# Kernel tuning notes

Measured on AMD Instinct MI355X. Metric: run time of the kernel, lower is better.

## Reference

```python
import jax, jax.numpy as jnp
import numpy as np

K_NN = 20  # neighbors per group (k=20 in source)


def fps_one(xyz, npoint):
    # xyz: [N,3] -> indices [npoint] via iterative furthest point sampling
    N = xyz.shape[0]
    def body(carry, _):
        dist, far = carry
        d = jnp.sum((xyz - xyz[far]) ** 2, axis=-1)
        dist = jnp.minimum(dist, d)
        return (dist, jnp.argmax(dist).astype(jnp.int32)), far
    init = (jnp.full((N,), 1e10, xyz.dtype), jnp.int32(0))
    _, idx = jax.lax.scan(body, init, None, length=npoint)
    return idx


def gather(pts, idx):
    # pts: [B,M,C], idx: [B,...] -> [B,...,C]
    return jax.vmap(lambda p, i: p[i])(pts, idx)


def knn(q, ref, k):
    # q: [B,S,3], ref: [B,M,3] -> [B,S,k] indices of nearest refs
    d = (jnp.sum(q * q, -1, keepdims=True)
         - 2.0 * jnp.einsum('bsc,bmc->bsm', q, ref)
         + jnp.sum(ref * ref, -1)[:, None, :])
    _, idx = jax.lax.top_k(-d, k)
    return idx


def sa_block(xyz, feats, npoint, W, b):
    # Set abstraction: FPS sample -> kNN group -> shared MLP -> max pool
    fidx = jax.vmap(fps_one, in_axes=(0, None))(xyz, npoint)   # [B,S]
    new_xyz = gather(xyz, fidx)                                 # [B,S,3]
    nidx = knn(new_xyz, xyz, K_NN)                              # [B,S,K]
    rel = gather(xyz, nidx) - new_xyz[:, :, None, :]            # [B,S,K,3]
    grp = jnp.concatenate([rel, gather(feats, nidx)], -1)       # [B,S,K,3+C]
    h = jax.nn.relu(jnp.einsum('bskc,cd->bskd', grp, W) + b)
    return new_xyz, jnp.max(h, axis=2)                          # [B,S,Cout]


def fp_block(xq, xr, fr, skip, W, b):
    # Feature propagation: 3-NN inverse-distance interp -> concat skip -> MLP
    idx = knn(xq, xr, 3)                                        # [B,S,3]
    d = jnp.sum((gather(xr, idx) - xq[:, :, None, :]) ** 2, -1)
    w = 1.0 / (d + 1e-8)
    w = w / jnp.sum(w, -1, keepdims=True)
    interp = jnp.einsum('bsk,bskc->bsc', w, gather(fr, idx))
    cat = jnp.concatenate([interp, skip], -1)
    return jax.nn.relu(jnp.einsum('bsc,cd->bsd', cat, W) + b)


def setup_inputs() -> dict:
    key = jax.random.key(0)
    ks = jax.random.split(key, 24)
    B, N = 8, 4096
    x = jax.random.normal(ks[0], (B, 6, N), jnp.float32)
    cls_label = jax.random.uniform(ks[1], (B, 16), jnp.float32)
    def lin(k, cin, cout):
        kw, kb = jax.random.split(k)
        s = 1.0 / np.sqrt(cin)
        return (jax.random.normal(kw, (cin, cout), jnp.float32) * s,
                jax.random.normal(kb, (cout,), jnp.float32) * 0.01)
    W0, b0 = lin(ks[2], 6, 64)
    W1, b1 = lin(ks[3], 67, 128)
    W2, b2 = lin(ks[4], 131, 256)
    W3, b3 = lin(ks[5], 259, 512)
    F3, fb3 = lin(ks[6], 768, 512)
    F2, fb2 = lin(ks[7], 640, 256)
    F1, fb1 = lin(ks[8], 320, 128)
    F0, fb0 = lin(ks[9], 150, 128)
    Wseg, bseg = lin(ks[10], 128, 50)
    return {"x": x, "cls_label": cls_label,
            "W0": W0, "b0": b0, "W1": W1, "b1": b1, "W2": W2, "b2": b2,
            "W3": W3, "b3": b3, "F3": F3, "fb3": fb3, "F2": F2, "fb2": fb2,
            "F1": F1, "fb1": fb1, "F0": F0, "fb0": fb0,
            "Wseg": Wseg, "bseg": bseg}


def reference(x, cls_label, W0, b0, W1, b1, W2, b2, W3, b3,
              F3, fb3, F2, fb2, F1, fb1, F0, fb0, Wseg, bseg):
    B, _, N = x.shape
    xyz = jnp.transpose(x[:, :3, :], (0, 2, 1))   # [B,N,3]
    nrm = jnp.transpose(x[:, 3:, :], (0, 2, 1))   # [B,N,3]
    # hierarchical set abstraction (512 -> 256 -> 128 -> 64 points)
    x1, f1 = sa_block(xyz, nrm, 512, W0, b0)      # f1: [B,512,64]
    x2, f2 = sa_block(x1, f1, 256, W1, b1)        # f2: [B,256,128]
    x3, f3 = sa_block(x2, f2, 128, W2, b2)        # f3: [B,128,256]
    x4, f4 = sa_block(x3, f3, 64, W3, b3)         # f4: [B,64,512]
    # feature propagation back up
    g3 = fp_block(x3, x4, f4, f3, F3, fb3)        # [B,128,512]
    g2 = fp_block(x2, x3, g3, f2, F2, fb2)        # [B,256,256]
    g1 = fp_block(x1, x2, g2, f1, F1, fb1)        # [B,512,128]
    cls = jnp.broadcast_to(cls_label[:, None, :], (B, N, 16))
    skip0 = jnp.concatenate([cls, xyz, nrm], -1)  # [B,N,22]
    g0 = fp_block(xyz, x1, g1, skip0, F0, fb0)    # [B,N,128]
    result = jnp.einsum('bnc,cd->bnd', g0, Wseg) + bseg  # [B,N,50]
    return result, jnp.transpose(g0, (0, 2, 1))
```

## Files before the change

### kernel.cpp

```cpp
#include <hip/hip_runtime.h>
#include <float.h>

#define B8 8
#define NPTS 4096

__global__ void split_xyz_kernel(const float* __restrict__ x,
                                 float* __restrict__ xyz, float* __restrict__ nrm) {
  int g = blockIdx.x * 256 + threadIdx.x;
  if (g >= B8 * NPTS) return;
  int b = g / NPTS, n = g % NPTS;
  const float* xb = x + (size_t)b * 6 * NPTS;
  float* o1 = xyz + (size_t)g * 3;
  float* o2 = nrm + (size_t)g * 3;
  o1[0] = xb[0 * NPTS + n]; o1[1] = xb[1 * NPTS + n]; o1[2] = xb[2 * NPTS + n];
  o2[0] = xb[3 * NPTS + n]; o2[1] = xb[4 * NPTS + n]; o2[2] = xb[5 * NPTS + n];
}

template <int CTRL, int RM>
__device__ __forceinline__ unsigned dppmov(unsigned v) {
  return (unsigned)__builtin_amdgcn_update_dpp((int)v, (int)v, CTRL, RM, 0xf, false);
}

template <int CTRL, int RM>
__device__ __forceinline__ void red_key_max(unsigned& kh, unsigned& kl) {
  unsigned oh = dppmov<CTRL, RM>(kh);
  unsigned ol = dppmov<CTRL, RM>(kl);
  unsigned long long ko = ((unsigned long long)oh << 32) | ol;
  unsigned long long k  = ((unsigned long long)kh << 32) | kl;
  bool c = ko > k;
  kh = c ? oh : kh;
  kl = c ? ol : kl;
}

template <int CTRL, int RM>
__device__ __forceinline__ void red_key_min(unsigned& kh, unsigned& kl) {
  unsigned oh = dppmov<CTRL, RM>(kh);
  unsigned ol = dppmov<CTRL, RM>(kl);
  unsigned long long ko = ((unsigned long long)oh << 32) | ol;
  unsigned long long k  = ((unsigned long long)kh << 32) | kl;
  bool c = ko < k;
  kh = c ? oh : kh;
  kl = c ? ol : kl;
}

#define WAVE_RED_MAX(kh, kl)            \
  red_key_max<0x111, 0xf>(kh, kl);      \
  red_key_max<0x112, 0xf>(kh, kl);      \
  red_key_max<0x114, 0xf>(kh, kl);      \
  red_key_max<0x118, 0xf>(kh, kl);      \
  red_key_max<0x142, 0xa>(kh, kl);      \
  red_key_max<0x143, 0xc>(kh, kl);

#define WAVE_RED_MIN(kh, kl)            \
  red_key_min<0x111, 0xf>(kh, kl);      \
  red_key_min<0x112, 0xf>(kh, kl);      \
  red_key_min<0x114, 0xf>(kh, kl);      \
  red_key_min<0x118, 0xf>(kh, kl);      \
  red_key_min<0x142, 0xa>(kh, kl);      \
  red_key_min<0x143, 0xc>(kh, kl);

template <int BLOCK, int P>
__global__ __launch_bounds__(BLOCK) void fps4_kernel(const float* __restrict__ xyz,
                                                     int N, int S,
                                                     float* __restrict__ out_xyz) {
#pragma clang fp contract(off)
  constexpr int NW = BLOCK / 64;
  __shared__ float4 pts[BLOCK * P];
  __shared__ float4 sel[512];
  __shared__ alignas(16) unsigned long long wkey[2][NW];
  int b = blockIdx.x, t = threadIdx.x;
  const float* p = xyz + (size_t)b * N * 3;
  float px[P], py[P], pz[P], dist[P];
#pragma unroll
  for (int j = 0; j < P; ++j) {
    int idx = t + j * BLOCK;
    float a = p[3 * idx], bb = p[3 * idx + 1], c = p[3 * idx + 2];
    px[j] = a; py[j] = bb; pz[j] = c;
    pts[idx] = make_float4(a, bb, c, 0.f);
    dist[j] = 1e10f;
  }
  __syncthreads();
  float fx = p[0], fy = p[1], fz = p[2];
  for (int i = 0; i < S; ++i) {
    if (t == 0) sel[i] = make_float4(fx, fy, fz, 0.f);
    float bv = -1.0f;
    int bj = 0;
#pragma unroll
    for (int j = 0; j < P; ++j) {
      float dx = px[j] - fx, dy = py[j] - fy, dz = pz[j] - fz;
      float d = dx * dx + dy * dy + dz * dz;
      float nd = fminf(dist[j], d);
      dist[j] = nd;
      bool c = nd > bv;
      bv = c ? nd : bv;
      bj = c ? j : bj;
    }
    unsigned kh = __float_as_uint(bv);
    unsigned kl = (unsigned)(~(t + bj * BLOCK));
    WAVE_RED_MAX(kh, kl);
    int buf = i & 1;
    if ((t & 63) == 63)
      wkey[buf][t >> 6] = ((unsigned long long)kh << 32) | kl;
    __syncthreads();
    unsigned long long g = 0ull;
    const ulonglong2* wk2 = (const ulonglong2*)&wkey[buf][0];
#pragma unroll
    for (int w = 0; w < NW / 2; ++w) {
      ulonglong2 e = wk2[w];
      unsigned long long m = (e.x > e.y) ? e.x : e.y;
      g = (m > g) ? m : g;
    }
    int far = (int)~(unsigned)g;
    float4 f = pts[far];
    fx = f.x; fy = f.y; fz = f.z;
  }
  __syncthreads();
  for (int i = t; i < S; i += BLOCK) {
    float4 f = sel[i];
    float* o = out_xyz + ((size_t)b * S + i) * 3;
    o[0] = f.x; o[1] = f.y; o[2] = f.z;
  }
}

__global__ __launch_bounds__(64) void knn20_kernel(const float* __restrict__ q,
                                                   const float* __restrict__ ref,
                                                   int S, int M, int* __restrict__ nidx,
                                                   int LDQ, int LDR) {
#pragma clang fp contract(off)
  int bs = blockIdx.x;
  int b = bs / S, s = bs % S;
  int t = threadIdx.x;
  __shared__ float sd[4096];
  const float* qp = q + ((size_t)b * LDQ + s) * 3;
  float qx = qp[0], qy = qp[1], qz = qp[2];
  float qq = qx * qx + qy * qy + qz * qz;
  const float* rp = ref + (size_t)b * LDR * 3;
  for (int i = t; i < M; i += 64) {
    float rx = rp[3 * i], ry = rp[3 * i + 1], rz = rp[3 * i + 2];
    float rr = rx * rx + ry * ry + rz * rz;
    float dot = qx * rx + qy * ry + qz * rz;
    sd[i] = qq - 2.0f * dot + rr;
  }
  __syncthreads();
  unsigned keep = 0;
  for (int k = 0; k < 20; ++k) {
    float bv = FLT_MAX;
    int bi = 0;
    for (int i = t; i < M; i += 64) {
      float v = sd[i];
      bool c = v < bv;
      bv = c ? v : bv;
      bi = c ? i : bi;
    }
    unsigned kh = __float_as_uint(bv), kl = (unsigned)bi;
    WAVE_RED_MIN(kh, kl);
    unsigned w = (unsigned)__builtin_amdgcn_readlane((int)kl, 63);
    if (t == k) keep = w;
    if (t == 0) sd[w] = FLT_MAX;
    __syncthreads();
  }
  if (t < 20) nidx[(size_t)bs * 20 + t] = (int)keep;
}

__device__ __forceinline__ void knn3_store(int g, const float* rx3,
                                           float qx, float qy, float qz,
                                           int i0, int i1, int i2,
                                           int* __restrict__ idx3,
                                           float* __restrict__ w3) {
#pragma clang fp contract(off)
  int ii[3] = {i0, i1, i2};
  float w[3];
  float wsum = 0.0f;
#pragma unroll
  for (int k = 0; k < 3; ++k) {
    const float* r = rx3 + (size_t)ii[k] * 3;
    float dx = r[0] - qx, dy = r[1] - qy, dz = r[2] - qz;
    float d = dx * dx + dy * dy + dz * dz;
    w[k] = 1.0f / (d + 1e-8f);
    wsum += w[k];
  }
#pragma unroll
  for (int k = 0; k < 3; ++k) {
    idx3[(size_t)g * 3 + k] = ii[k];
    w3[(size_t)g * 3 + k] = w[k] / wsum;
  }
}

__global__ __launch_bounds__(256) void neighbors_kernel(
    const float* __restrict__ xyz, const float* __restrict__ x1,
    int* __restrict__ nidx2, int* __restrict__ nidx3, int* __restrict__ nidx4,
    int* __restrict__ idx3_3, float* __restrict__ w3_3,
    int* __restrict__ idx3_2, float* __restrict__ w3_2,
    int* __restrict__ idx3_1, float* __restrict__ w3_1,
    int* __restrict__ idx3_0, float* __restrict__ w3_0) {
#pragma clang fp contract(off)
  __shared__ float4 smem4[512];
  int blk = blockIdx.x, tid = threadIdx.x;

  if (blk < 896) {
    int S, M, qid;
    int* nout;
    const int wv = tid >> 6, t64 = tid & 63;
    if (blk < 512)      { S = 256; M = 512; qid = blk * 4 + wv;         nout = nidx2; }
    else if (blk < 768) { S = 128; M = 256; qid = (blk - 512) * 4 + wv; nout = nidx3; }
    else                { S = 64;  M = 128; qid = (blk - 768) * 4 + wv; nout = nidx4; }
    float* swd = (float*)smem4 + wv * M;
    int b = qid / S, s = qid % S;
    const float* qp = x1 + ((size_t)b * 512 + s) * 3;
    float qx = qp[0], qy = qp[1], qz = qp[2];
    float qq = qx * qx + qy * qy + qz * qz;
    const float* rp = x1 + (size_t)b * 512 * 3;
    for (int i = t64; i < M; i += 64) {
      float rx = rp[3 * i], ry = rp[3 * i + 1], rz = rp[3 * i + 2];
      float rr = rx * rx + ry * ry + rz * rz;
      float dot = qx * rx + qy * ry + qz * rz;
      swd[i] = qq - 2.0f * dot + rr;
    }
    __syncthreads();
    unsigned keep = 0;
    for (int k = 0; k < 20; ++k) {
      float bv = FLT_MAX;
      int bi = 0;
      for (int i = t64; i < M; i += 64) {
        float v = swd[i];
        bool c = v < bv;
        bv = c ? v : bv;
        bi = c ? i : bi;
      }
      unsigned kh = __float_as_uint(bv), kl = (unsigned)bi;
      WAVE_RED_MIN(kh, kl);
      unsigned w = (unsigned)__builtin_amdgcn_readlane((int)kl, 63);
      if (t64 == k) keep = w;
      if (t64 == 0) swd[w] = FLT_MAX;
      __syncthreads();
    }
    if (t64 < 20) nout[(size_t)qid * 20 + t64] = (int)keep;
    return;
  }

  if (blk < 900) {
    int g = (blk - 896) * 256 + tid;
    int Sq = 128, M = 64;
    int b = g / Sq, s = g % Sq;
    const float* qp = x1 + ((size_t)b * 512 + s) * 3;
    float qx = qp[0], qy = qp[1], qz = qp[2];
    float qq = qx * qx + qy * qy + qz * qz;
    const float* rp = x1 + (size_t)b * 512 * 3;
    float v0 = FLT_MAX, v1 = FLT_MAX, v2 = FLT_MAX;
    int i0 = 0, i1 = 0, i2 = 0;
    for (int i = 0; i < M; ++i) {
      float rx = rp[3 * i], ry = rp[3 * i + 1], rz = rp[3 * i + 2];
      float d = qq - 2.0f * (qx * rx + qy * ry + qz * rz) + (rx * rx + ry * ry + rz * rz);
      if (d < v2) {
        if (d < v1) {
          if (d < v0) { v2 = v1; i2 = i1; v1 = v0; i1 = i0; v0 = d; i0 = i; }
          else { v2 = v1; i2 = i1; v1 = d; i1 = i; }
        } else { v2 = d; i2 = i; }
      }
    }
    knn3_store(g, rp, qx, qy, qz, i0, i1, i2, idx3_3, w3_3);
    return;
  }

  int g, Sq, M, LDQ;
  int* oidx;
  float* ow;
  const float* q;
  if (blk < 908)      { g = (blk - 900) * 256 + tid; Sq = 256;  M = 128; oidx = idx3_2; ow = w3_2; q = x1;  LDQ = 512; }
  else if (blk < 924) { g = (blk - 908) * 256 + tid; Sq = 512;  M = 256; oidx = idx3_1; ow = w3_1; q = x1;  LDQ = 512; }
  else                { g = (blk - 924) * 256 + tid; Sq = 4096; M = 512; oidx = idx3_0; ow = w3_0; q = xyz; LDQ = 4096; }
  int b = g / Sq, s = g % Sq;
  const float* rp = x1 + (size_t)b * 512 * 3;
  for (int i = tid; i < M; i += 256) {
    float rx = rp[3 * i], ry = rp[3 * i + 1], rz = rp[3 * i + 2];
    smem4[i] = make_float4(rx, ry, rz, rx * rx + ry * ry + rz * rz);
  }
  __syncthreads();
  const float* qp = q + ((size_t)b * LDQ + s) * 3;
  float qx = qp[0], qy = qp[1], qz = qp[2];
  float qq = qx * qx + qy * qy + qz * qz;
  float v0 = FLT_MAX, v1 = FLT_MAX, v2 = FLT_MAX;
  int i0 = 0, i1 = 0, i2 = 0;
  for (int i = 0; i < M; ++i) {
    float4 r = smem4[i];
    float d = qq - 2.0f * (qx * r.x + qy * r.y + qz * r.z) + r.w;
    if (d < v2) {
      if (d < v1) {
        if (d < v0) { v2 = v1; i2 = i1; v1 = v0; i1 = i0; v0 = d; i0 = i; }
        else { v2 = v1; i2 = i1; v1 = d; i1 = i; }
      } else { v2 = d; i2 = i; }
    }
  }
  {
    int ii[3] = {i0, i1, i2};
    float w[3];
    float wsum = 0.0f;
#pragma unroll
    for (int k = 0; k < 3; ++k) {
      float4 r = smem4[ii[k]];
      float dx = r.x - qx, dy = r.y - qy, dz = r.z - qz;
      float d = dx * dx + dy * dy + dz * dz;
      w[k] = 1.0f / (d + 1e-8f);
      wsum += w[k];
    }
#pragma unroll
    for (int k = 0; k < 3; ++k) {
      oidx[(size_t)g * 3 + k] = ii[k];
      ow[(size_t)g * 3 + k] = w[k] / wsum;
    }
  }
}

#define GEMM_STAGE(k0v, ...)                                                      \
    _Pragma("unroll")                                                             \
    for (int u = 0; u < 4; ++u) {                                                 \
      int l = (int)threadIdx.x + u * 256;                                         \
      int m = l >> 4, kk = l & 15;                                                \
      int rr = rowBase + m, kq = (k0v) + kk;                                      \
      float v = 0.0f;                                                             \
      if (rr < Mrows && kq < K) { __VA_ARGS__ }                                   \
      areg[u] = v;                                                                \
    }                                                                             \
    _Pragma("unroll")                                                             \
    for (int u = 0; u < 4; ++u) {                                                 \
      int l = (int)threadIdx.x + u * 256;                                         \
      int kk = l >> 6, n = l & 63;                                                \
      int kq = (k0v) + kk, cc = colBase + n;                                      \
      breg[u] = (kq < K && cc < N) ? Wm[(size_t)kq * N + cc] : 0.0f;              \
    }

#define GEMM_WRITE_LDS(bufv)                                                      \
    _Pragma("unroll")                                                             \
    for (int u = 0; u < 4; ++u) {                                                 \
      int l = (int)threadIdx.x + u * 256;                                         \
      As[bufv][l & 15][l >> 4] = areg[u];                                         \
    }                                                                             \
    _Pragma("unroll")                                                             \
    for (int u = 0; u < 4; ++u) {                                                 \
      int l = (int)threadIdx.x + u * 256;                                         \
      Bs[bufv][l >> 6][l & 63] = breg[u];                                         \
    }

#define GEMM_MAIN(...)                                                            \
  __shared__ alignas(16) float As[2][16][68];                                     \
  __shared__ float Bs[2][16][64];                                                 \
  int tx = threadIdx.x & 15, ty = threadIdx.x >> 4;                               \
  int rowBase = blockIdx.y * 64;                                                  \
  int colBase = blockIdx.x * 64;                                                  \
  float acc[4][4] = {};                                                           \
  float areg[4], breg[4];                                                         \
  GEMM_STAGE(0, __VA_ARGS__)                                                      \
  GEMM_WRITE_LDS(0)                                                               \
  __syncthreads();                                                                \
  int cur = 0;                                                                    \
  for (int k0 = 0; k0 < K; k0 += 16) {                                            \
    int nxt = cur ^ 1;                                                            \
    bool more = (k0 + 16 < K);                                                    \
    if (more) { GEMM_STAGE(k0 + 16, __VA_ARGS__) }                                \
    _Pragma("unroll")                                                             \
    for (int kk = 0; kk < 16; ++kk) {                                             \
      const float4 av = *reinterpret_cast<const float4*>(&As[cur][kk][ty * 4]);   \
      const float4 bv = *reinterpret_cast<const float4*>(&Bs[cur][kk][tx * 4]);   \
      acc[0][0] += av.x * bv.x; acc[0][1] += av.x * bv.y;                         \
      acc[0][2] += av.x * bv.z; acc[0][3] += av.x * bv.w;                         \
      acc[1][0] += av.y * bv.x; acc[1][1] += av.y * bv.y;                         \
      acc[1][2] += av.y * bv.z; acc[1][3] += av.y * bv.w;                         \
      acc[2][0] += av.z * bv.x; acc[2][1] += av.z * bv.y;                         \
      acc[2][2] += av.z * bv.z; acc[2][3] += av.z * bv.w;                         \
      acc[3][0] += av.w * bv.x; acc[3][1] += av.w * bv.y;                         \
      acc[3][2] += av.w * bv.z; acc[3][3] += av.w * bv.w;                         \
    }                                                                             \
    if (more) { GEMM_WRITE_LDS(nxt) }                                             \
    __syncthreads();                                                              \
    cur = nxt;                                                                    \
  }

#define GEMM_EPI_STORE                                                            \
  _Pragma("unroll")                                                               \
  for (int i = 0; i < 4; ++i) {                                                   \
    int row = rowBase + ty * 4 + i;                                               \
    if (row >= Mrows) continue;                                                   \
    _Pragma("unroll")                                                             \
    for (int j = 0; j < 4; ++j) {                                                 \
      int col = colBase + tx * 4 + j;                                             \
      if (col >= N) continue;                                                     \
      float v = acc[i][j] + bias[col];                                            \
      if (RELU) v = fmaxf(v, 0.0f);                                               \
      C[(size_t)row * N + col] = v;                                               \
    }                                                                             \
  }

__global__ __launch_bounds__(256) void gemm_kernel(const float* __restrict__ A,
                                                   const float* __restrict__ Wm,
                                                   const float* __restrict__ bias,
                                                   float* __restrict__ C,
                                                   int Mrows, int N, int K, int RELU) {
  GEMM_MAIN( v = A[(size_t)rr * K + kq]; )
  GEMM_EPI_STORE
}

__global__ __launch_bounds__(256) void gemm_sa_kernel(
    const float* __restrict__ xyz, const float* __restrict__ feats,
    const float* __restrict__ new_xyz, const int* __restrict__ nidx,
    const float* __restrict__ Wm, const float* __restrict__ bias,
    float* __restrict__ fOut, int Mref, int LDR, int S, int LDQ, int Cf,
    int Mrows, int N, int K) {
  GEMM_MAIN(
    int bs = rr / 20;
    int s_ = bs % S;
    int b = bs / S;
    int id = nidx[rr];
    if (kq < 3)
      v = xyz[((size_t)b * LDR + id) * 3 + kq] - new_xyz[((size_t)b * LDQ + s_) * 3 + kq];
    else
      v = feats[((size_t)b * Mref + id) * Cf + (kq - 3)];
  )
  __shared__ int smax[4][64];
  int gBase = rowBase / 20;
  int nG = (rowBase + 63) / 20 - gBase + 1;
  for (int l = threadIdx.x; l < nG * 64; l += 256) smax[l >> 6][l & 63] = 0;
  __syncthreads();
#pragma unroll
  for (int i = 0; i < 4; ++i) {
    int row = rowBase + ty * 4 + i;
    if (row >= Mrows) continue;
    int gl = row / 20 - gBase;
#pragma unroll
    for (int j = 0; j < 4; ++j) {
      int col = colBase + tx * 4 + j;
      if (col >= N) continue;
      float v = fmaxf(acc[i][j] + bias[col], 0.0f);
      atomicMax(&smax[gl][col - colBase], __float_as_int(v));
    }
  }
  __syncthreads();
  for (int l = threadIdx.x; l < nG * 64; l += 256) {
    int g = gBase + (l >> 6), c = colBase + (l & 63);
    if (c < N) atomicMax((int*)&fOut[(size_t)g * N + c], smax[l >> 6][l & 63]);
  }
}

__global__ __launch_bounds__(256) void gemm_fp_kernel(
    const float* __restrict__ fr, const int* __restrict__ idx3,
    const float* __restrict__ w3, const float* __restrict__ skip,
    const float* __restrict__ cls, const float* __restrict__ xyzq,
    const float* __restrict__ nrmq,
    const float* __restrict__ Wm, const float* __restrict__ bias,
    float* __restrict__ C, int Sq, int Mr, int Cr, int Cs, int mode,
    int Mrows, int N, int K) {
  const int RELU = 1;
  GEMM_MAIN(
    int bs = rr;
    int b = bs / Sq;
    if (kq < Cr) {
      const int* ii = idx3 + (size_t)bs * 3;
      const float* ww = w3 + (size_t)bs * 3;
      const float* fb = fr + (size_t)b * Mr * Cr;
      v = ww[0] * fb[(size_t)ii[0] * Cr + kq];
      v += ww[1] * fb[(size_t)ii[1] * Cr + kq];
      v += ww[2] * fb[(size_t)ii[2] * Cr + kq];
    } else {
      int cc = kq - Cr;
      if (mode == 0) {
        v = skip[(size_t)bs * Cs + cc];
      } else {
        if (cc < 16) v = cls[(size_t)b * 16 + cc];
        else if (cc < 19) v = xyzq[(size_t)bs * 3 + (cc - 16)];
        else v = nrmq[(size_t)bs * 3 + (cc - 19)];
      }
    }
  )
  GEMM_EPI_STORE
}

__global__ __launch_bounds__(256) void transpose_g0_kernel(const float* __restrict__ g0,
                                                           float* __restrict__ out2) {
  __shared__ float tile[32][33];
  int n0 = blockIdx.x * 32, c0 = blockIdx.y * 32, b = blockIdx.z;
  int tx = threadIdx.x & 31, ty = threadIdx.x >> 5;
#pragma unroll
  for (int j = 0; j < 32; j += 8)
    tile[ty + j][tx] = g0[((size_t)b * NPTS + n0 + ty + j) * 128 + c0 + tx];
  __syncthreads();
#pragma unroll
  for (int j = 0; j < 32; j += 8)
    out2[((size_t)b * 128 + c0 + ty + j) * NPTS + n0 + tx] = tile[tx][ty + j];
}

static inline int cdiv(int a, int b) { return (a + b - 1) / b; }

extern "C" void kernel_launch(void* const* d_in, const int* in_sizes, int n_in,
                              void* d_out, int out_size, void* d_ws, size_t ws_size,
                              hipStream_t stream) {
  const float* x    = (const float*)d_in[0];
  const float* cls  = (const float*)d_in[1];
  const float* W0 = (const float*)d_in[2];  const float* b0 = (const float*)d_in[3];
  const float* W1 = (const float*)d_in[4];  const float* b1 = (const float*)d_in[5];
  const float* W2 = (const float*)d_in[6];  const float* b2 = (const float*)d_in[7];
  const float* W3 = (const float*)d_in[8];  const float* b3 = (const float*)d_in[9];
  const float* F3 = (const float*)d_in[10]; const float* fb3 = (const float*)d_in[11];
  const float* F2 = (const float*)d_in[12]; const float* fb2 = (const float*)d_in[13];
  const float* F1 = (const float*)d_in[14]; const float* fb1 = (const float*)d_in[15];
  const float* F0 = (const float*)d_in[16]; const float* fb0 = (const float*)d_in[17];
  const float* Wseg = (const float*)d_in[18]; const float* bseg = (const float*)d_in[19];
  float* out = (float*)d_out;

  float* ws = (float*)d_ws;
  size_t off = 0;
  auto alloc = [&](size_t n) { float* p = ws + off; off += (n + 3) & ~(size_t)3; return p; };
  float* xyz = alloc(8 * 4096 * 3);
  float* nrm = alloc(8 * 4096 * 3);
  float* x1 = alloc(8 * 512 * 3);
  float* f1 = alloc(8 * 512 * 64);
  float* f2 = alloc(8 * 256 * 128);
  float* f3 = alloc(8 * 128 * 256);
  float* f4 = alloc(8 * 64 * 512);
  float* g3 = alloc(8 * 128 * 512);
  float* g2 = alloc(8 * 256 * 256);
  float* g1 = alloc(8 * 512 * 128);
  float* g0 = alloc(8 * 4096 * 128);
  int* nidx1 = (int*)alloc(8 * 512 * 20);
  int* nidx2 = (int*)alloc(8 * 256 * 20);
  int* nidx3 = (int*)alloc(8 * 128 * 20);
  int* nidx4 = (int*)alloc(8 * 64 * 20);
  int* idx3_3 = (int*)alloc(8 * 128 * 3);  float* w3_3 = alloc(8 * 128 * 3);
  int* idx3_2 = (int*)alloc(8 * 256 * 3);  float* w3_2 = alloc(8 * 256 * 3);
  int* idx3_1 = (int*)alloc(8 * 512 * 3);  float* w3_1 = alloc(8 * 512 * 3);
  int* idx3_0 = (int*)alloc(8 * 4096 * 3); float* w3_0 = alloc(8 * 4096 * 3);

  hipMemsetAsync(f1, 0, (size_t)8 * (512 * 64 + 256 * 128 + 128 * 256 + 64 * 512) * 4, stream);

  split_xyz_kernel<<<cdiv(8 * 4096, 256), 256, 0, stream>>>(x, xyz, nrm);
  fps4_kernel<256, 16><<<8, 256, 0, stream>>>(xyz, 4096, 512, x1);
  knn20_kernel<<<8 * 512, 64, 0, stream>>>(x1, xyz, 512, 4096, nidx1, 512, 4096);
  neighbors_kernel<<<1052, 256, 0, stream>>>(xyz, x1, nidx2, nidx3, nidx4,
                                             idx3_3, w3_3, idx3_2, w3_2,
                                             idx3_1, w3_1, idx3_0, w3_0);

  {
    dim3 grid(1, cdiv(8 * 512 * 20, 64));
    gemm_sa_kernel<<<grid, 256, 0, stream>>>(xyz, nrm, x1, nidx1, W0, b0, f1,
                                             4096, 4096, 512, 512, 3,
                                             8 * 512 * 20, 64, 6);
  }
  {
    dim3 grid(2, cdiv(8 * 256 * 20, 64));
    gemm_sa_kernel<<<grid, 256, 0, stream>>>(x1, f1, x1, nidx2, W1, b1, f2,
                                             512, 512, 256, 512, 64,
                                             8 * 256 * 20, 128, 67);
  }
  {
    dim3 grid(4, cdiv(8 * 128 * 20, 64));
    gemm_sa_kernel<<<grid, 256, 0, stream>>>(x1, f2, x1, nidx3, W2, b2, f3,
                                             256, 512, 128, 512, 128,
                                             8 * 128 * 20, 256, 131);
  }
  {
    dim3 grid(8, cdiv(8 * 64 * 20, 64));
    gemm_sa_kernel<<<grid, 256, 0, stream>>>(x1, f3, x1, nidx4, W3, b3, f4,
                                             128, 512, 64, 512, 256,
                                             8 * 64 * 20, 512, 259);
  }

  {
    dim3 grid(8, cdiv(8 * 128, 64));
    gemm_fp_kernel<<<grid, 256, 0, stream>>>(f4, idx3_3, w3_3, f3, nullptr, nullptr, nullptr,
                                             F3, fb3, g3, 128, 64, 512, 256, 0,
                                             8 * 128, 512, 768);
  }
  {
    dim3 grid(4, cdiv(8 * 256, 64));
    gemm_fp_kernel<<<grid, 256, 0, stream>>>(g3, idx3_2, w3_2, f2, nullptr, nullptr, nullptr,
                                             F2, fb2, g2, 256, 128, 512, 128, 0,
                                             8 * 256, 256, 640);
  }
  {
    dim3 grid(2, cdiv(8 * 512, 64));
    gemm_fp_kernel<<<grid, 256, 0, stream>>>(g2, idx3_1, w3_1, f1, nullptr, nullptr, nullptr,
                                             F1, fb1, g1, 512, 256, 256, 64, 0,
                                             8 * 512, 128, 320);
  }
  {
    dim3 grid(2, cdiv(8 * 4096, 64));
    gemm_fp_kernel<<<grid, 256, 0, stream>>>(g1, idx3_0, w3_0, nullptr, cls, xyz, nrm,
                                             F0, fb0, g0, 4096, 512, 128, 22, 1,
                                             8 * 4096, 128, 150);
  }

  {
    dim3 grid(1, cdiv(8 * 4096, 64));
    gemm_kernel<<<grid, 256, 0, stream>>>(g0, Wseg, bseg, out, 8 * 4096, 50, 128, 0);
  }
  transpose_g0_kernel<<<dim3(128, 4, 8), 256, 0, stream>>>(g0, out + (size_t)8 * 4096 * 50);
}
```

Before: 1.124 ms.

## Process two batches per block in FPS to interleave independent reductions

The furthest point sampling kernel now handles two batch elements per block, and the grid shrinks from 8 to 4 blocks. Both batches' distance updates and wave reductions are interleaved and share one barrier per iteration. This is meant to hide the reduction and shared-memory latency of the serial FPS loop and to halve the barrier count per batch. In exchange, each block does twice the arithmetic per iteration and uses twice the registers and shared memory, with fewer blocks running in parallel.

```diff
diff --git a/kernel.cpp b/kernel.cpp
--- a/kernel.cpp
+++ b/kernel.cpp
@@ -60,65 +60,116 @@
   red_key_min<0x143, 0xc>(kh, kl);
 
 template <int BLOCK, int P>
-__global__ __launch_bounds__(BLOCK) void fps4_kernel(const float* __restrict__ xyz,
-                                                     int N, int S,
-                                                     float* __restrict__ out_xyz) {
+__global__ __launch_bounds__(BLOCK) void fps4x2_kernel(const float* __restrict__ xyz,
+                                                       int N, int S,
+                                                       float* __restrict__ out_xyz) {
 #pragma clang fp contract(off)
   constexpr int NW = BLOCK / 64;
-  __shared__ float4 pts[BLOCK * P];
-  __shared__ float4 sel[512];
-  __shared__ alignas(16) unsigned long long wkey[2][NW];
-  int b = blockIdx.x, t = threadIdx.x;
-  const float* p = xyz + (size_t)b * N * 3;
-  float px[P], py[P], pz[P], dist[P];
+  __shared__ float4 ptsA[BLOCK * P];
+  __shared__ float4 ptsB[BLOCK * P];
+  __shared__ float4 selA[512];
+  __shared__ float4 selB[512];
+  __shared__ alignas(16) unsigned long long wkey[2][2][NW];
+  int b0 = blockIdx.x * 2, t = threadIdx.x;
+  const float* pA = xyz + (size_t)b0 * N * 3;
+  const float* pB = xyz + (size_t)(b0 + 1) * N * 3;
+  float pxA[P], pyA[P], pzA[P], dsA[P];
+  float pxB[P], pyB[P], pzB[P], dsB[P];
 #pragma unroll
   for (int j = 0; j < P; ++j) {
     int idx = t + j * BLOCK;
-    float a = p[3 * idx], bb = p[3 * idx + 1], c = p[3 * idx + 2];
-    px[j] = a; py[j] = bb; pz[j] = c;
-    pts[idx] = make_float4(a, bb, c, 0.f);
-    dist[j] = 1e10f;
+    float ax = pA[3 * idx], ay = pA[3 * idx + 1], az = pA[3 * idx + 2];
+    pxA[j] = ax; pyA[j] = ay; pzA[j] = az;
+    ptsA[idx] = make_float4(ax, ay, az, 0.f);
+    dsA[j] = 1e10f;
+    float bx = pB[3 * idx], by = pB[3 * idx + 1], bz = pB[3 * idx + 2];
+    pxB[j] = bx; pyB[j] = by; pzB[j] = bz;
+    ptsB[idx] = make_float4(bx, by, bz, 0.f);
+    dsB[j] = 1e10f;
   }
   __syncthreads();
-  float fx = p[0], fy = p[1], fz = p[2];
+  float fxA = pA[0], fyA = pA[1], fzA = pA[2];
+  float fxB = pB[0], fyB = pB[1], fzB = pB[2];
   for (int i = 0; i < S; ++i) {
-    if (t == 0) sel[i] = make_float4(fx, fy, fz, 0.f);
-    float bv = -1.0f;
-    int bj = 0;
-#pragma unroll
-    for (int j = 0; j < P; ++j) {
-      float dx = px[j] - fx, dy = py[j] - fy, dz = pz[j] - fz;
-      float d = dx * dx + dy * dy + dz * dz;
-      float nd = fminf(dist[j], d);
-      dist[j] = nd;
-      bool c = nd > bv;
-      bv = c ? nd : bv;
-      bj = c ? j : bj;
-    }
-    unsigned kh = __float_as_uint(bv);
-    unsigned kl = (unsigned)(~(t + bj * BLOCK));
-    WAVE_RED_MAX(kh, kl);
+    if (t == 0) {
+      selA[i] = make_float4(fxA, fyA, fzA, 0.f);
+      selB[i] = make_float4(fxB, fyB, fzB, 0.f);
+    }
     int buf = i & 1;
-    if ((t & 63) == 63)
-      wkey[buf][t >> 6] = ((unsigned long long)kh << 32) | kl;
+    {
+      float bv = -1.0f;
+      int bj = 0;
+#pragma unroll
+      for (int j = 0; j < P; ++j) {
+        float dx = pxA[j] - fxA, dy = pyA[j] - fyA, dz = pzA[j] - fzA;
+        float d = dx * dx + dy * dy + dz * dz;
+        float nd = fminf(dsA[j], d);
+        dsA[j] = nd;
+        bool c = nd > bv;
+        bv = c ? nd : bv;
+        bj = c ? j : bj;
+      }
+      unsigned kh = __float_as_uint(bv);
+      unsigned kl = (unsigned)(~(t + bj * BLOCK));
+      WAVE_RED_MAX(kh, kl);
+      if ((t & 63) == 63)
+        wkey[buf][0][t >> 6] = ((unsigned long long)kh << 32) | kl;
+    }
+    {
+      float bv = -1.0f;
+      int bj = 0;
+#pragma unroll
+      for (int j = 0; j < P; ++j) {
+        float dx = pxB[j] - fxB, dy = pyB[j] - fyB, dz = pzB[j] - fzB;
+        float d = dx * dx + dy * dy + dz * dz;
+        float nd = fminf(dsB[j], d);
+        dsB[j] = nd;
+        bool c = nd > bv;
+        bv = c ? nd : bv;
+        bj = c ? j : bj;
+      }
+      unsigned kh = __float_as_uint(bv);
+      unsigned kl = (unsigned)(~(t + bj * BLOCK));
+      WAVE_RED_MAX(kh, kl);
+      if ((t & 63) == 63)
+        wkey[buf][1][t >> 6] = ((unsigned long long)kh << 32) | kl;
+    }
     __syncthreads();
-    unsigned long long g = 0ull;
-    const ulonglong2* wk2 = (const ulonglong2*)&wkey[buf][0];
-#pragma unroll
-    for (int w = 0; w < NW / 2; ++w) {
-      ulonglong2 e = wk2[w];
-      unsigned long long m = (e.x > e.y) ? e.x : e.y;
-      g = (m > g) ? m : g;
-    }
-    int far = (int)~(unsigned)g;
-    float4 f = pts[far];
-    fx = f.x; fy = f.y; fz = f.z;
+    {
+      unsigned long long g = 0ull;
+      const ulonglong2* wk2 = (const ulonglong2*)&wkey[buf][0][0];
+#pragma unroll
+      for (int w = 0; w < NW / 2; ++w) {
+        ulonglong2 e = wk2[w];
+        unsigned long long m = (e.x > e.y) ? e.x : e.y;
+        g = (m > g) ? m : g;
+      }
+      int far = (int)~(unsigned)g;
+      float4 f = ptsA[far];
+      fxA = f.x; fyA = f.y; fzA = f.z;
+    }
+    {
+      unsigned long long g = 0ull;
+      const ulonglong2* wk2 = (const ulonglong2*)&wkey[buf][1][0];
+#pragma unroll
+      for (int w = 0; w < NW / 2; ++w) {
+        ulonglong2 e = wk2[w];
+        unsigned long long m = (e.x > e.y) ? e.x : e.y;
+        g = (m > g) ? m : g;
+      }
+      int far = (int)~(unsigned)g;
+      float4 f = ptsB[far];
+      fxB = f.x; fyB = f.y; fzB = f.z;
+    }
   }
   __syncthreads();
   for (int i = t; i < S; i += BLOCK) {
-    float4 f = sel[i];
-    float* o = out_xyz + ((size_t)b * S + i) * 3;
-    o[0] = f.x; o[1] = f.y; o[2] = f.z;
+    float4 a = selA[i];
+    float* oa = out_xyz + ((size_t)b0 * S + i) * 3;
+    oa[0] = a.x; oa[1] = a.y; oa[2] = a.z;
+    float4 bq = selB[i];
+    float* ob = out_xyz + ((size_t)(b0 + 1) * S + i) * 3;
+    ob[0] = bq.x; ob[1] = bq.y; ob[2] = bq.z;
   }
 }
 
@@ -531,7 +582,7 @@
   hipMemsetAsync(f1, 0, (size_t)8 * (512 * 64 + 256 * 128 + 128 * 256 + 64 * 512) * 4, stream);
 
   split_xyz_kernel<<<cdiv(8 * 4096, 256), 256, 0, stream>>>(x, xyz, nrm);
-  fps4_kernel<256, 16><<<8, 256, 0, stream>>>(xyz, 4096, 512, x1);
+  fps4x2_kernel<256, 16><<<4, 256, 0, stream>>>(xyz, 4096, 512, x1);
   knn20_kernel<<<8 * 512, 64, 0, stream>>>(x1, xyz, 512, 4096, nidx1, 512, 4096);
   neighbors_kernel<<<1052, 256, 0, stream>>>(xyz, x1, nidx2, nidx3, nidx4,
                                              idx3_3, w3_3, idx3_2, w3_2,
```

Result: slower. 1.394 ms (+24.1%).

## Split-K the FP GEMMs with atomics and defer bias+ReLU to the consumer

Applied to the files above, without the earlier changes.

Splits the K dimension of the first three feature-propagation GEMMs across blockIdx.z and accumulates partial sums with atomicAdd into zero-initialised outputs, which raises block count on these small-M layers. Because partial sums cannot have bias and ReLU applied, those are deferred and applied to the gathered inputs of the next FP layer via a new frBias argument. It also vectorises the weight-tile load and LDS store to float4. This adds atomic traffic, a larger memset, and nondeterministic summation order.

```diff
diff --git a/kernel.cpp b/kernel.cpp
--- a/kernel.cpp
+++ b/kernel.cpp
@@ -321,12 +321,19 @@
       if (rr < Mrows && kq < K) { __VA_ARGS__ }                                   \
       areg[u] = v;                                                                \
     }                                                                             \
-    _Pragma("unroll")                                                             \
-    for (int u = 0; u < 4; ++u) {                                                 \
-      int l = (int)threadIdx.x + u * 256;                                         \
-      int kk = l >> 6, n = l & 63;                                                \
-      int kq = (k0v) + kk, cc = colBase + n;                                      \
-      breg[u] = (kq < K && cc < N) ? Wm[(size_t)kq * N + cc] : 0.0f;              \
+    {                                                                             \
+      int kk = (int)threadIdx.x >> 4;                                             \
+      int n4 = ((int)threadIdx.x & 15) * 4;                                       \
+      int kq = (k0v) + kk, cc = colBase + n4;                                     \
+      if (colBase + 64 <= N) {                                                    \
+        if (kq < K) breg4 = *reinterpret_cast<const float4*>(&Wm[(size_t)kq * N + cc]); \
+        else breg4 = make_float4(0.f, 0.f, 0.f, 0.f);                             \
+      } else {                                                                    \
+        breg4.x = (kq < K && cc < N) ? Wm[(size_t)kq * N + cc] : 0.0f;            \
+        breg4.y = (kq < K && cc + 1 < N) ? Wm[(size_t)kq * N + cc + 1] : 0.0f;    \
+        breg4.z = (kq < K && cc + 2 < N) ? Wm[(size_t)kq * N + cc + 2] : 0.0f;    \
+        breg4.w = (kq < K && cc + 3 < N) ? Wm[(size_t)kq * N + cc + 3] : 0.0f;    \
+      }                                                                           \
     }
 
 #define GEMM_WRITE_LDS(bufv)                                                      \
@@ -335,27 +342,24 @@
       int l = (int)threadIdx.x + u * 256;                                         \
       As[bufv][l & 15][l >> 4] = areg[u];                                         \
     }                                                                             \
-    _Pragma("unroll")                                                             \
-    for (int u = 0; u < 4; ++u) {                                                 \
-      int l = (int)threadIdx.x + u * 256;                                         \
-      Bs[bufv][l >> 6][l & 63] = breg[u];                                         \
-    }
+    *reinterpret_cast<float4*>(&Bs[bufv][threadIdx.x >> 4][(threadIdx.x & 15) * 4]) = breg4;
 
 #define GEMM_MAIN(...)                                                            \
   __shared__ alignas(16) float As[2][16][68];                                     \
-  __shared__ float Bs[2][16][64];                                                 \
+  __shared__ alignas(16) float Bs[2][16][64];                                     \
   int tx = threadIdx.x & 15, ty = threadIdx.x >> 4;                               \
   int rowBase = blockIdx.y * 64;                                                  \
   int colBase = blockIdx.x * 64;                                                  \
   float acc[4][4] = {};                                                           \
-  float areg[4], breg[4];                                                         \
-  GEMM_STAGE(0, __VA_ARGS__)                                                      \
+  float areg[4];                                                                  \
+  float4 breg4;                                                                   \
+  GEMM_STAGE(kLo, __VA_ARGS__)                                                    \
   GEMM_WRITE_LDS(0)                                                               \
   __syncthreads();                                                                \
   int cur = 0;                                                                    \
-  for (int k0 = 0; k0 < K; k0 += 16) {                                            \
+  for (int k0 = kLo; k0 < kHi; k0 += 16) {                                        \
     int nxt = cur ^ 1;                                                            \
-    bool more = (k0 + 16 < K);                                                    \
+    bool more = (k0 + 16 < kHi);                                                  \
     if (more) { GEMM_STAGE(k0 + 16, __VA_ARGS__) }                                \
     _Pragma("unroll")                                                             \
     for (int kk = 0; kk < 16; ++kk) {                                             \
@@ -395,6 +399,7 @@
                                                    const float* __restrict__ bias,
                                                    float* __restrict__ C,
                                                    int Mrows, int N, int K, int RELU) {
+  const int kLo = 0, kHi = K;
   GEMM_MAIN( v = A[(size_t)rr * K + kq]; )
   GEMM_EPI_STORE
 }
@@ -405,6 +410,7 @@
     const float* __restrict__ Wm, const float* __restrict__ bias,
     float* __restrict__ fOut, int Mref, int LDR, int S, int LDQ, int Cf,
     int Mrows, int N, int K) {
+  const int kLo = 0, kHi = K;
   GEMM_MAIN(
     int bs = rr / 20;
     int s_ = bs % S;
@@ -444,11 +450,13 @@
     const float* __restrict__ fr, const int* __restrict__ idx3,
     const float* __restrict__ w3, const float* __restrict__ skip,
     const float* __restrict__ cls, const float* __restrict__ xyzq,
-    const float* __restrict__ nrmq,
+    const float* __restrict__ nrmq, const float* __restrict__ frBias,
     const float* __restrict__ Wm, const float* __restrict__ bias,
     float* __restrict__ C, int Sq, int Mr, int Cr, int Cs, int mode,
+    int SPLITK, int CHUNK,
     int Mrows, int N, int K) {
-  const int RELU = 1;
+  const int kLo = blockIdx.z * CHUNK;
+  const int kHi = min(K, kLo + CHUNK);
   GEMM_MAIN(
     int bs = rr;
     int b = bs / Sq;
@@ -456,9 +464,16 @@
       const int* ii = idx3 + (size_t)bs * 3;
       const float* ww = w3 + (size_t)bs * 3;
       const float* fb = fr + (size_t)b * Mr * Cr;
-      v = ww[0] * fb[(size_t)ii[0] * Cr + kq];
-      v += ww[1] * fb[(size_t)ii[1] * Cr + kq];
-      v += ww[2] * fb[(size_t)ii[2] * Cr + kq];
+      float a0 = fb[(size_t)ii[0] * Cr + kq];
+      float a1 = fb[(size_t)ii[1] * Cr + kq];
+      float a2 = fb[(size_t)ii[2] * Cr + kq];
+      if (frBias) {
+        float bb = frBias[kq];
+        a0 = fmaxf(a0 + bb, 0.0f);
+        a1 = fmaxf(a1 + bb, 0.0f);
+        a2 = fmaxf(a2 + bb, 0.0f);
+      }
+      v = ww[0] * a0 + ww[1] * a1 + ww[2] * a2;
     } else {
       int cc = kq - Cr;
       if (mode == 0) {
@@ -470,7 +485,22 @@
       }
     }
   )
-  GEMM_EPI_STORE
+  if (SPLITK) {
+#pragma unroll
+    for (int i = 0; i < 4; ++i) {
+      int row = rowBase + ty * 4 + i;
+      if (row >= Mrows) continue;
+#pragma unroll
+      for (int j = 0; j < 4; ++j) {
+        int col = colBase + tx * 4 + j;
+        if (col >= N) continue;
+        atomicAdd(&C[(size_t)row * N + col], acc[i][j]);
+      }
+    }
+  } else {
+    const int RELU = 1;
+    GEMM_EPI_STORE
+  }
 }
 
 __global__ __launch_bounds__(256) void transpose_g0_kernel(const float* __restrict__ g0,
@@ -528,7 +558,9 @@
   int* idx3_1 = (int*)alloc(8 * 512 * 3);  float* w3_1 = alloc(8 * 512 * 3);
   int* idx3_0 = (int*)alloc(8 * 4096 * 3); float* w3_0 = alloc(8 * 4096 * 3);
 
-  hipMemsetAsync(f1, 0, (size_t)8 * (512 * 64 + 256 * 128 + 128 * 256 + 64 * 512) * 4, stream);
+  hipMemsetAsync(f1, 0,
+                 ((size_t)8 * (512 * 64 + 256 * 128 + 128 * 256 + 64 * 512) +
+                  (size_t)8 * (128 * 512 + 256 * 256 + 512 * 128)) * 4, stream);
 
   split_xyz_kernel<<<cdiv(8 * 4096, 256), 256, 0, stream>>>(x, xyz, nrm);
   fps4_kernel<256, 16><<<8, 256, 0, stream>>>(xyz, 4096, 512, x1);
@@ -563,28 +595,28 @@
   }
 
   {
-    dim3 grid(8, cdiv(8 * 128, 64));
+    dim3 grid(8, cdiv(8 * 128, 64), 4);
     gemm_fp_kernel<<<grid, 256, 0, stream>>>(f4, idx3_3, w3_3, f3, nullptr, nullptr, nullptr,
-                                             F3, fb3, g3, 128, 64, 512, 256, 0,
-                                             8 * 128, 512, 768);
-  }
-  {
-    dim3 grid(4, cdiv(8 * 256, 64));
+                                             nullptr, F3, fb3, g3, 128, 64, 512, 256, 0,
+                                             1, 192, 8 * 128, 512, 768);
+  }
+  {
+    dim3 grid(4, cdiv(8 * 256, 64), 4);
     gemm_fp_kernel<<<grid, 256, 0, stream>>>(g3, idx3_2, w3_2, f2, nullptr, nullptr, nullptr,
-                                             F2, fb2, g2, 256, 128, 512, 128, 0,
-                                             8 * 256, 256, 640);
-  }
-  {
-    dim3 grid(2, cdiv(8 * 512, 64));
+                                             fb3, F2, fb2, g2, 256, 128, 512, 128, 0,
+                                             1, 160, 8 * 256, 256, 640);
+  }
+  {
+    dim3 grid(2, cdiv(8 * 512, 64), 2);
     gemm_fp_kernel<<<grid, 256, 0, stream>>>(g2, idx3_1, w3_1, f1, nullptr, nullptr, nullptr,
-                                             F1, fb1, g1, 512, 256, 256, 64, 0,
-                                             8 * 512, 128, 320);
-  }
-  {
-    dim3 grid(2, cdiv(8 * 4096, 64));
+                                             fb2, F1, fb1, g1, 512, 256, 256, 64, 0,
+                                             1, 160, 8 * 512, 128, 320);
+  }
+  {
+    dim3 grid(2, cdiv(8 * 4096, 64), 1);
     gemm_fp_kernel<<<grid, 256, 0, stream>>>(g1, idx3_0, w3_0, nullptr, cls, xyz, nrm,
-                                             F0, fb0, g0, 4096, 512, 128, 22, 1,
-                                             8 * 4096, 128, 150);
+                                             fb1, F0, fb0, g0, 4096, 512, 128, 22, 1,
+                                             0, 160, 8 * 4096, 128, 150);
   }
 
   {
```

New measurement: 1.060 ms. -5.6%, faster.
